# Kernel optimization log

Hardware: AMD Instinct MI355X
Metric: run time of the kernel (lower is better)

Reference implementation:

```python
import jax, jax.numpy as jnp
import numpy as np

N, E, G = 50000, 800000, 64        # nodes, edges, graphs in batch
IN, HID, OUT = 64, 128, 8


def gcn_conv(x, W, b, src, dst, num_nodes):
    """GCNConv: h = D^-1/2 (A+I) D^-1/2 (x W) + b, self-loops already in src/dst."""
    h = x @ W                                              # [N, out]
    deg = jax.ops.segment_sum(jnp.ones_like(dst, dtype=h.dtype), dst,
                              num_segments=num_nodes)      # [N]
    dinv = jax.lax.rsqrt(jnp.maximum(deg, 1.0))
    norm = dinv[src] * dinv[dst]                           # [E+N]
    msg = h[src] * norm[:, None]                           # gather + scale
    out = jax.ops.segment_sum(msg, dst, num_segments=num_nodes)
    return out + b


def global_mean_pool(x, batch, num_graphs):
    s = jax.ops.segment_sum(x, batch, num_segments=num_graphs)
    cnt = jax.ops.segment_sum(jnp.ones((x.shape[0],), x.dtype), batch,
                              num_segments=num_graphs)
    return s / jnp.maximum(cnt, 1.0)[:, None]


def setup_inputs() -> dict:
    key = jax.random.key(0)
    ks = jax.random.split(key, 11)
    def glorot(k, fi, fo):
        return jax.random.normal(k, (fi, fo), jnp.float32) * np.float32(1.0 / np.sqrt(fi))
    return {
        "x": jax.random.normal(ks[0], (N, IN), jnp.float32),
        "W1": glorot(ks[1], IN, HID),  "b1": jnp.zeros((HID,), jnp.float32),
        "W2": glorot(ks[2], HID, HID), "b2": jnp.zeros((HID,), jnp.float32),
        "W3": glorot(ks[3], HID, HID), "b3": jnp.zeros((HID,), jnp.float32),
        "Wh": glorot(ks[4], HID, OUT), "bh": jnp.zeros((OUT,), jnp.float32),
        "edge_index": jax.random.randint(ks[5], (2, E), 0, N),
        "batch": jnp.sort(jax.random.randint(ks[6], (N,), 0, G)),
    }


def reference(x, W1, b1, W2, b2, W3, b3, Wh, bh, edge_index, batch):
    loops = jnp.arange(N, dtype=edge_index.dtype)
    src = jnp.concatenate([edge_index[0], loops])          # add self-loops
    dst = jnp.concatenate([edge_index[1], loops])
    h = jax.nn.relu(gcn_conv(x, W1, b1, src, dst, N))
    h = jax.nn.relu(gcn_conv(h, W2, b2, src, dst, N))
    h = gcn_conv(h, W3, b3, src, dst, N)
    g = global_mean_pool(h, batch, G)                      # [G, HID]
    return g @ Wh + bh                                     # [G, OUT]
```

## Files before the change

kernel.cpp:

```cpp
#include <hip/hip_runtime.h>

typedef short bf8_t __attribute__((ext_vector_type(8)));
typedef float f32x4 __attribute__((ext_vector_type(4)));
typedef unsigned short u16;

__device__ inline u16 f2bf(float f) {
    unsigned u = __float_as_uint(f);
    return (u16)((u + 0x7fff + ((u >> 16) & 1)) >> 16);
}


__global__ void deg_kernel(const int* __restrict__ dst, int* __restrict__ deg,
                           u16* __restrict__ rank, int E) {
    int e = blockIdx.x * 256 + threadIdx.x;
    if (e < E) rank[e] = (u16)atomicAdd(&deg[dst[e]], 1);
}

__global__ void scan_blocksum(const int* __restrict__ deg, int* __restrict__ bsum,
                              float* __restrict__ dinv, int n) {
    int i = blockIdx.x * 256 + threadIdx.x;
    int d = (i < n) ? (deg[i] + 1) : 0;
    if (i < n) dinv[i] = rsqrtf((float)d);
    int v = (i < n) ? ((d + 7) & ~7) : 0;
    for (int off = 32; off > 0; off >>= 1) v += __shfl_down(v, off, 64);
    __shared__ int ws[4];
    if ((threadIdx.x & 63) == 0) ws[threadIdx.x >> 6] = v;
    __syncthreads();
    if (threadIdx.x == 0) bsum[blockIdx.x] = ws[0] + ws[1] + ws[2] + ws[3];
}

__global__ void scan_offsets(const int* __restrict__ bsum, int* __restrict__ boff, int nblk) {
    __shared__ int buf[256];
    int tid = threadIdx.x;
    int v = (tid < nblk) ? bsum[tid] : 0;
    buf[tid] = v;
    __syncthreads();
    for (int off = 1; off < 256; off <<= 1) {
        int t = (tid >= off) ? buf[tid - off] : 0;
        __syncthreads();
        buf[tid] += t;
        __syncthreads();
    }
    if (tid < nblk) boff[tid] = buf[tid] - v;
}

__global__ void scan_rowptr(const int* __restrict__ deg, const int* __restrict__ boff,
                            int* __restrict__ row_ptr, int n) {
    __shared__ int buf[256];
    int tid = threadIdx.x;
    int i = blockIdx.x * 256 + tid;
    int v = (i < n) ? ((deg[i] + 8) & ~7) : 0;
    buf[tid] = v;
    __syncthreads();
    for (int off = 1; off < 256; off <<= 1) {
        int t = (tid >= off) ? buf[tid - off] : 0;
        __syncthreads();
        buf[tid] += t;
        __syncthreads();
    }
    int excl = buf[tid] - v + boff[blockIdx.x];
    if (i < n) row_ptr[i] = excl;
    if (i == n - 1) row_ptr[n] = excl + v;
}


__global__ void prep_kernel(const int* __restrict__ src, const int* __restrict__ dst,
                            const u16* __restrict__ rank, const int* __restrict__ row_ptr,
                            const int* __restrict__ deg,
                            u16* __restrict__ csr_src,
                            const float* __restrict__ x, const float* __restrict__ dinv,
                            unsigned* __restrict__ x16, unsigned* __restrict__ h16a,
                            unsigned* __restrict__ h16b,
                            const float* __restrict__ W1, const float* __restrict__ W2,
                            const float* __restrict__ W3,
                            u16* __restrict__ Wt1, u16* __restrict__ Wt2,
                            u16* __restrict__ Wt3,
                            int E, int n, int total8) {
    int gid = blockIdx.x * 256 + threadIdx.x;
    if (gid < E) {
        int s = src[gid], d = dst[gid];
        int pos = row_ptr[d] + 1 + (int)rank[gid];
        __builtin_nontemporal_store((u16)s, &csr_src[pos]);
        return;
    }
    if (gid < E + n) {
        int s = gid - E;
        int beg = row_ptr[s];
        csr_src[beg] = (u16)s;
        int fill0 = beg + deg[s] + 1, fill1 = row_ptr[s + 1];
        for (int p = fill0; p < fill1; ++p) csr_src[p] = (u16)n;
        return;
    }
    int i = gid - (E + n);
    if (i < total8) {
        float dn = dinv[i >> 3];
        const float4* x4 = (const float4*)x;
        float4 a = x4[i * 2], b = x4[i * 2 + 1];
        uint4 o;
        o.x = (unsigned)f2bf(a.x * dn) | ((unsigned)f2bf(a.y * dn) << 16);
        o.y = (unsigned)f2bf(a.z * dn) | ((unsigned)f2bf(a.w * dn) << 16);
        o.z = (unsigned)f2bf(b.x * dn) | ((unsigned)f2bf(b.y * dn) << 16);
        o.w = (unsigned)f2bf(b.z * dn) | ((unsigned)f2bf(b.w * dn) << 16);
        ((uint4*)x16)[i] = o;
        return;
    }
    int j = i - total8;
    if (j < 8192) {
        int nn = j / 64, k = j - nn * 64;
        Wt1[j] = f2bf(W1[k * 128 + nn]);
        return;
    }
    if (j < 24576) {
        int jj = j - 8192;
        int nn = jj / 128, k = jj - nn * 128;
        Wt2[jj] = f2bf(W2[k * 128 + nn]);
        return;
    }
    if (j < 40960) {
        int jj = j - 24576;
        int nn = jj / 128, k = jj - nn * 128;
        Wt3[jj] = f2bf(W3[k * 128 + nn]);
        return;
    }
    int z = j - 40960;
    if (z < 8)       x16 [(size_t)n * 32 + z]  = 0u;
    else if (z < 16) ((uint4*)x16)[(size_t)n * 8 + (z - 8)] = make_uint4(0,0,0,0);
    else if (z < 32) ((uint4*)h16a)[(size_t)n * 16 + (z - 16)] = make_uint4(0,0,0,0);
    else if (z < 48) ((uint4*)h16b)[(size_t)n * 16 + (z - 32)] = make_uint4(0,0,0,0);
}


__device__ inline void bf8_add(uint4 a, float* acc) {
#pragma unroll
    for (int j = 0; j < 4; ++j) {
        unsigned u = ((const unsigned*)&a)[j];
        acc[2 * j]     += __uint_as_float(u << 16);
        acc[2 * j + 1] += __uint_as_float(u & 0xffff0000u);
    }
}

__device__ inline uint4 pack_bf8(const float* v, float dn) {
    uint4 o;
    o.x = (unsigned)f2bf(v[0] * dn) | ((unsigned)f2bf(v[1] * dn) << 16);
    o.y = (unsigned)f2bf(v[2] * dn) | ((unsigned)f2bf(v[3] * dn) << 16);
    o.z = (unsigned)f2bf(v[4] * dn) | ((unsigned)f2bf(v[5] * dn) << 16);
    o.w = (unsigned)f2bf(v[6] * dn) | ((unsigned)f2bf(v[7] * dn) << 16);
    return o;
}

template<int K, bool RELU, bool BF16OUT>
__global__ __launch_bounds__(256) void agg_gemm(
        const u16* __restrict__ in, const u16* __restrict__ Wt16,
        const float* __restrict__ bias, void* __restrict__ outp,
        const int* __restrict__ row_ptr, const u16* __restrict__ csr_src,
        const float* __restrict__ dinv, int n) {
    constexpr int KS = K / 32;
    __shared__ u16 As[16 * K];
    int w = threadIdx.x >> 6, lane = threadIdx.x & 63;
    int base = blockIdx.x * 16;
    int lr = lane & 15, lk = lane >> 4;

    bf8_t B[2][KS];
#pragma unroll
    for (int f = 0; f < 2; ++f) {
        int col = w * 32 + f * 16 + lr;
#pragma unroll
        for (int ks = 0; ks < KS; ++ks)
            B[f][ks] = *reinterpret_cast<const bf8_t*>(&Wt16[(size_t)col * K + ks * 32 + lk * 8]);
    }

    const uint4* in4 = (const uint4*)in;
    int g = lane >> 4;
    int row = w * 4 + g;
    int node = base + row;
    float acc[8] = {0.f, 0.f, 0.f, 0.f, 0.f, 0.f, 0.f, 0.f};

    if (K == 128) {
        int col = lane & 15;
        if (node < n) {
            int beg = row_ptr[node];
            int niter = (row_ptr[node + 1] - beg) >> 3;
            const uint4* idxp = (const uint4*)(csr_src + beg);
            uint4 iv = idxp[0];
            for (int it = 0; it < niter; ++it) {
                uint4 ivn = idxp[it + 1];
                int s0 = iv.x & 0xffff, s1 = iv.x >> 16;
                int s2 = iv.y & 0xffff, s3 = iv.y >> 16;
                int s4 = iv.z & 0xffff, s5 = iv.z >> 16;
                int s6 = iv.w & 0xffff, s7 = iv.w >> 16;
                uint4 a0 = in4[(size_t)s0 * 16 + col];
                uint4 a1 = in4[(size_t)s1 * 16 + col];
                uint4 a2 = in4[(size_t)s2 * 16 + col];
                uint4 a3 = in4[(size_t)s3 * 16 + col];
                bf8_add(a0, acc); bf8_add(a1, acc);
                bf8_add(a2, acc); bf8_add(a3, acc);
                uint4 a4 = in4[(size_t)s4 * 16 + col];
                uint4 a5 = in4[(size_t)s5 * 16 + col];
                uint4 a6 = in4[(size_t)s6 * 16 + col];
                uint4 a7 = in4[(size_t)s7 * 16 + col];
                bf8_add(a4, acc); bf8_add(a5, acc);
                bf8_add(a6, acc); bf8_add(a7, acc);
                iv = ivn;
            }
        }
        float dn = (node < n) ? dinv[node] : 0.f;
        int off = row * K + ((col * 8) ^ ((row & 7) << 3));
        *(uint4*)&As[off] = pack_bf8(acc, dn);
    } else {
        int sub = (lane >> 3) & 1;
        int col = lane & 7;
        if (node < n) {
            int beg = row_ptr[node];
            int niter = (row_ptr[node + 1] - beg) >> 3;
            const uint4* idxp = (const uint4*)(csr_src + beg);
            uint4 iv = idxp[0];
            for (int it = 0; it < niter; ++it) {
                uint4 ivn = idxp[it + 1];
                int e0 = sub ? (int)(iv.x >> 16) : (int)(iv.x & 0xffff);
                int e1 = sub ? (int)(iv.y >> 16) : (int)(iv.y & 0xffff);
                int e2 = sub ? (int)(iv.z >> 16) : (int)(iv.z & 0xffff);
                int e3 = sub ? (int)(iv.w >> 16) : (int)(iv.w & 0xffff);
                uint4 a0 = in4[(size_t)e0 * 8 + col];
                uint4 a1 = in4[(size_t)e1 * 8 + col];
                uint4 a2 = in4[(size_t)e2 * 8 + col];
                uint4 a3 = in4[(size_t)e3 * 8 + col];
                bf8_add(a0, acc); bf8_add(a1, acc);
                bf8_add(a2, acc); bf8_add(a3, acc);
                iv = ivn;
            }
        }
#pragma unroll
        for (int j = 0; j < 8; ++j)
            acc[j] += __shfl_xor(acc[j], 8, 64);
        if (sub == 0) {
            float dn = (node < n) ? dinv[node] : 0.f;
            int off = row * K + ((col * 8) ^ ((row & 7) << 3));
            *(uint4*)&As[off] = pack_bf8(acc, dn);
        }
    }
    __syncthreads();

    f32x4 pacc[2] = {};
#pragma unroll
    for (int ks = 0; ks < KS; ++ks) {
        int off = lr * K + (((ks * 32) + lk * 8) ^ ((lr & 7) << 3));
        bf8_t a = *reinterpret_cast<const bf8_t*>(&As[off]);
#pragma unroll
        for (int f = 0; f < 2; ++f)
            pacc[f] = __builtin_amdgcn_mfma_f32_16x16x32_bf16(B[f][ks], a, pacc[f], 0, 0, 0);
    }

    int orow = base + lr;
    if (orow < n) {
        float dnx = BF16OUT ? dinv[orow] : 1.f;
#pragma unroll
        for (int f = 0; f < 2; ++f) {
            int c0 = w * 32 + f * 16 + lk * 4;
            float4 bv = *(const float4*)&bias[c0];
            float v0 = pacc[f][0] + bv.x, v1 = pacc[f][1] + bv.y;
            float v2 = pacc[f][2] + bv.z, v3 = pacc[f][3] + bv.w;
            if (RELU) {
                v0 = fmaxf(v0, 0.f); v1 = fmaxf(v1, 0.f);
                v2 = fmaxf(v2, 0.f); v3 = fmaxf(v3, 0.f);
            }
            if (BF16OUT) {
                uint2 o;
                o.x = (unsigned)f2bf(v0 * dnx) | ((unsigned)f2bf(v1 * dnx) << 16);
                o.y = (unsigned)f2bf(v2 * dnx) | ((unsigned)f2bf(v3 * dnx) << 16);
                *(uint2*)&((u16*)outp)[(size_t)orow * 128 + c0] = o;
            } else {
                *(float4*)&((float*)outp)[(size_t)orow * 128 + c0] = make_float4(v0, v1, v2, v3);
            }
        }
    }
}


__device__ inline int lbound(const int* __restrict__ batch, int n, int g) {
    int lo = 0, hi = n;
    while (lo < hi) {
        int mid = (lo + hi) >> 1;
        if (batch[mid] < g) lo = mid + 1; else hi = mid;
    }
    return lo;
}

#define PSPLIT 16
__global__ __launch_bounds__(256) void pool_part(
        const float* __restrict__ h, const int* __restrict__ batch,
        float* __restrict__ part, int n) {
    int g = blockIdx.x >> 4, sp = blockIdx.x & (PSPLIT - 1);
    int tid = threadIdx.x;
    int c = tid & 127, rs = tid >> 7;
    int beg = lbound(batch, n, g), end = lbound(batch, n, g + 1);
    int len = end - beg;
    int chunk = (len + PSPLIT - 1) >> 4;
    int r0 = beg + sp * chunk;
    int r1 = min(r0 + chunk, end);
    float acc = 0.f;
    for (int r = r0 + rs; r < r1; r += 2)
        acc += h[(size_t)r * 128 + c];
    __shared__ float buf[256];
    buf[tid] = acc;
    __syncthreads();
    if (rs == 0)
        part[(size_t)blockIdx.x * 128 + c] = buf[c] + buf[c + 128];
}

__global__ __launch_bounds__(128) void pool_head(
        const float* __restrict__ part, const int* __restrict__ batch,
        const float* __restrict__ Wh, const float* __restrict__ bh,
        float* __restrict__ out, int n) {
    int g = blockIdx.x;
    int tid = threadIdx.x;
    float acc = 0.f;
#pragma unroll
    for (int sp = 0; sp < PSPLIT; ++sp)
        acc += part[((size_t)g * PSPLIT + sp) * 128 + tid];
    int cnt = lbound(batch, n, g + 1) - lbound(batch, n, g);
    __shared__ float grow[128];
    grow[tid] = acc / fmaxf((float)cnt, 1.f);
    __syncthreads();
    int sub = tid >> 3, o = tid & 7;
    float p = 0.f;
    for (int k = sub; k < 128; k += 16)
        p += grow[k] * Wh[k * 8 + o];
    __shared__ float p2[128];
    p2[tid] = p;
    __syncthreads();
    for (int s = 8; s > 0; s >>= 1) {
        if (sub < s) p2[sub * 8 + o] += p2[(sub + s) * 8 + o];
        __syncthreads();
    }
    if (tid < 8) out[g * 8 + tid] = p2[tid] + bh[tid];
}


extern "C" void kernel_launch(void* const* d_in, const int* in_sizes, int n_in,
                              void* d_out, int out_size, void* d_ws, size_t ws_size,
                              hipStream_t stream) {
    const float* x  = (const float*)d_in[0];
    const float* W1 = (const float*)d_in[1];
    const float* b1 = (const float*)d_in[2];
    const float* W2 = (const float*)d_in[3];
    const float* b2 = (const float*)d_in[4];
    const float* W3 = (const float*)d_in[5];
    const float* b3 = (const float*)d_in[6];
    const float* Wh = (const float*)d_in[7];
    const float* bh = (const float*)d_in[8];
    const int* edge_index = (const int*)d_in[9];
    const int* batch = (const int*)d_in[10];
    (void)n_in; (void)ws_size;

    const int N = in_sizes[10];
    const int E = in_sizes[9] / 2;
    const int G = out_size / 8;
    const int* esrc = edge_index;
    const int* edst = edge_index + E;

    size_t off = 0;
    auto take = [&](size_t bytes) {
        void* p = (char*)d_ws + off;
        off += (bytes + 255) & ~(size_t)255;
        return p;
    };
    int*   deg      = (int*)take((size_t)N * 4);
    float* dinv     = (float*)take((size_t)N * 4);
    int*   row_ptr  = (int*)take((size_t)(N + 1) * 4);
    u16*   rank     = (u16*)take((size_t)E * 2);
    u16*   csr_src  = (u16*)take(((size_t)E + 8 * (size_t)N + 16) * 2);
    int*   bsum     = (int*)take(256 * 4);
    int*   boff     = (int*)take(256 * 4);
    float* part     = (float*)take((size_t)G * PSPLIT * 128 * 4);
    u16*   x16      = (u16*)take((size_t)(N + 1) * 64 * 2);
    u16*   h16a     = (u16*)take((size_t)(N + 1) * 128 * 2);
    u16*   h16b     = (u16*)take((size_t)(N + 1) * 128 * 2);
    u16*   Wt1      = (u16*)take((size_t)128 * 64 * 2);
    u16*   Wt2      = (u16*)take((size_t)128 * 128 * 2);
    u16*   Wt3      = (u16*)take((size_t)128 * 128 * 2);
    float* bufA     = (float*)take((size_t)N * 128 * 4);

    int nblk  = (N + 255) / 256;
    int fgrid = (N + 15) / 16;
    int total8 = N * 64 / 8;
    int prep_threads = E + N + total8 + 40960 + 64;

    hipMemsetAsync(deg, 0, (size_t)N * 4, stream);

    deg_kernel<<<(E + 255) / 256, 256, 0, stream>>>(edst, deg, rank, E);
    scan_blocksum<<<nblk, 256, 0, stream>>>(deg, bsum, dinv, N);
    scan_offsets<<<1, 256, 0, stream>>>(bsum, boff, nblk);
    scan_rowptr<<<nblk, 256, 0, stream>>>(deg, boff, row_ptr, N);
    prep_kernel<<<(prep_threads + 255) / 256, 256, 0, stream>>>(
        esrc, edst, rank, row_ptr, deg, csr_src, x, dinv,
        (unsigned*)x16, (unsigned*)h16a, (unsigned*)h16b,
        W1, W2, W3, Wt1, Wt2, Wt3, E, N, total8);

    agg_gemm<64,  true,  true ><<<fgrid, 256, 0, stream>>>(x16,  Wt1, b1, h16a, row_ptr, csr_src, dinv, N);
    agg_gemm<128, true,  true ><<<fgrid, 256, 0, stream>>>(h16a, Wt2, b2, h16b, row_ptr, csr_src, dinv, N);
    agg_gemm<128, false, false><<<fgrid, 256, 0, stream>>>(h16b, Wt3, b3, bufA, row_ptr, csr_src, dinv, N);

    pool_part<<<G * PSPLIT, 256, 0, stream>>>(bufA, batch, part, N);
    pool_head<<<G, 128, 0, stream>>>(part, batch, Wh, bh, (float*)d_out, N);
}
```

Before: 199.9 us.

## Fold layer-3 weight into head and replace final agg-GEMM with aggregation only

Since layer 3 has no activation and is followed by linear mean pooling and the head, W3 and Wh (and b3 into bh) are pre-multiplied into a 128x8 matrix. The last layer becomes a plain sparse aggregation that writes bf16 instead of fp32, and pooling reads bf16. This removes one dense MFMA GEMM and halves the final-layer write and pool read traffic. The cost is one extra bf16 rounding of the aggregated features and a small serial dot-product setup in the prep kernel.

```diff
diff --git a/kernel.cpp b/kernel.cpp
--- a/kernel.cpp
+++ b/kernel.cpp
@@ -73,8 +73,10 @@
                             unsigned* __restrict__ h16b,
                             const float* __restrict__ W1, const float* __restrict__ W2,
                             const float* __restrict__ W3,
+                            const float* __restrict__ Wh, const float* __restrict__ b3,
+                            const float* __restrict__ bh,
                             u16* __restrict__ Wt1, u16* __restrict__ Wt2,
-                            u16* __restrict__ Wt3,
+                            float* __restrict__ WhF, float* __restrict__ bhF,
                             int E, int n, int total8) {
     int gid = blockIdx.x * 256 + threadIdx.x;
     if (gid < E) {
@@ -116,17 +118,27 @@
         Wt2[jj] = f2bf(W2[k * 128 + nn]);
         return;
     }
-    if (j < 40960) {
+    if (j < 25600) {
         int jj = j - 24576;
-        int nn = jj / 128, k = jj - nn * 128;
-        Wt3[jj] = f2bf(W3[k * 128 + nn]);
-        return;
-    }
-    int z = j - 40960;
-    if (z < 8)       x16 [(size_t)n * 32 + z]  = 0u;
-    else if (z < 16) ((uint4*)x16)[(size_t)n * 8 + (z - 8)] = make_uint4(0,0,0,0);
-    else if (z < 32) ((uint4*)h16a)[(size_t)n * 16 + (z - 16)] = make_uint4(0,0,0,0);
-    else if (z < 48) ((uint4*)h16b)[(size_t)n * 16 + (z - 32)] = make_uint4(0,0,0,0);
+        int k = jj >> 3, o = jj & 7;
+        float a = 0.f;
+        for (int q = 0; q < 128; ++q)
+            a += W3[k * 128 + q] * Wh[q * 8 + o];
+        WhF[jj] = a;
+        return;
+    }
+    if (j < 25608) {
+        int o = j - 25600;
+        float a = bh[o];
+        for (int q = 0; q < 128; ++q)
+            a += b3[q] * Wh[q * 8 + o];
+        bhF[o] = a;
+        return;
+    }
+    int z = j - 25608;
+    if (z < 8)       ((uint4*)x16) [(size_t)n * 8  + z]        = make_uint4(0, 0, 0, 0);
+    else if (z < 24) ((uint4*)h16a)[(size_t)n * 16 + (z - 8)]  = make_uint4(0, 0, 0, 0);
+    else if (z < 40) ((uint4*)h16b)[(size_t)n * 16 + (z - 24)] = make_uint4(0, 0, 0, 0);
 }
 
 
@@ -147,6 +159,7 @@
     o.w = (unsigned)f2bf(v[6] * dn) | ((unsigned)f2bf(v[7] * dn) << 16);
     return o;
 }
+
 
 template<int K, bool RELU, bool BF16OUT>
 __global__ __launch_bounds__(256) void agg_gemm(
@@ -276,6 +289,45 @@
 }
 
 
+__global__ __launch_bounds__(256) void agg_only(
+        const u16* __restrict__ in, u16* __restrict__ out,
+        const int* __restrict__ row_ptr, const u16* __restrict__ csr_src,
+        const float* __restrict__ dinv, int n) {
+    int lane = threadIdx.x & 63;
+    int w = threadIdx.x >> 6;
+    int node = blockIdx.x * 16 + w * 4 + (lane >> 4);
+    int col = lane & 15;
+    if (node >= n) return;
+    const uint4* in4 = (const uint4*)in;
+    float acc[8] = {0.f, 0.f, 0.f, 0.f, 0.f, 0.f, 0.f, 0.f};
+    int beg = row_ptr[node];
+    int niter = (row_ptr[node + 1] - beg) >> 3;
+    const uint4* idxp = (const uint4*)(csr_src + beg);
+    uint4 iv = idxp[0];
+    for (int it = 0; it < niter; ++it) {
+        uint4 ivn = idxp[it + 1];
+        int s0 = iv.x & 0xffff, s1 = iv.x >> 16;
+        int s2 = iv.y & 0xffff, s3 = iv.y >> 16;
+        int s4 = iv.z & 0xffff, s5 = iv.z >> 16;
+        int s6 = iv.w & 0xffff, s7 = iv.w >> 16;
+        uint4 a0 = in4[(size_t)s0 * 16 + col];
+        uint4 a1 = in4[(size_t)s1 * 16 + col];
+        uint4 a2 = in4[(size_t)s2 * 16 + col];
+        uint4 a3 = in4[(size_t)s3 * 16 + col];
+        bf8_add(a0, acc); bf8_add(a1, acc);
+        bf8_add(a2, acc); bf8_add(a3, acc);
+        uint4 a4 = in4[(size_t)s4 * 16 + col];
+        uint4 a5 = in4[(size_t)s5 * 16 + col];
+        uint4 a6 = in4[(size_t)s6 * 16 + col];
+        uint4 a7 = in4[(size_t)s7 * 16 + col];
+        bf8_add(a4, acc); bf8_add(a5, acc);
+        bf8_add(a6, acc); bf8_add(a7, acc);
+        iv = ivn;
+    }
+    ((uint4*)out)[(size_t)node * 16 + col] = pack_bf8(acc, dinv[node]);
+}
+
+
 __device__ inline int lbound(const int* __restrict__ batch, int n, int g) {
     int lo = 0, hi = n;
     while (lo < hi) {
@@ -287,29 +339,38 @@
 
 #define PSPLIT 16
 __global__ __launch_bounds__(256) void pool_part(
-        const float* __restrict__ h, const int* __restrict__ batch,
+        const u16* __restrict__ v, const int* __restrict__ batch,
         float* __restrict__ part, int n) {
     int g = blockIdx.x >> 4, sp = blockIdx.x & (PSPLIT - 1);
     int tid = threadIdx.x;
-    int c = tid & 127, rs = tid >> 7;
+    int c2 = tid & 63;
+    int rs = tid >> 6;
     int beg = lbound(batch, n, g), end = lbound(batch, n, g + 1);
     int len = end - beg;
     int chunk = (len + PSPLIT - 1) >> 4;
     int r0 = beg + sp * chunk;
     int r1 = min(r0 + chunk, end);
-    float acc = 0.f;
-    for (int r = r0 + rs; r < r1; r += 2)
-        acc += h[(size_t)r * 128 + c];
-    __shared__ float buf[256];
-    buf[tid] = acc;
-    __syncthreads();
-    if (rs == 0)
-        part[(size_t)blockIdx.x * 128 + c] = buf[c] + buf[c + 128];
+    const unsigned* v32 = (const unsigned*)v;
+    float ax = 0.f, ay = 0.f;
+    for (int r = r0 + rs; r < r1; r += 4) {
+        unsigned u = v32[(size_t)r * 64 + c2];
+        ax += __uint_as_float(u << 16);
+        ay += __uint_as_float(u & 0xffff0000u);
+    }
+    __shared__ float bufx[256], bufy[256];
+    bufx[tid] = ax; bufy[tid] = ay;
+    __syncthreads();
+    if (rs == 0) {
+        float sx = bufx[c2] + bufx[c2 + 64] + bufx[c2 + 128] + bufx[c2 + 192];
+        float sy = bufy[c2] + bufy[c2 + 64] + bufy[c2 + 128] + bufy[c2 + 192];
+        part[(size_t)blockIdx.x * 128 + c2 * 2]     = sx;
+        part[(size_t)blockIdx.x * 128 + c2 * 2 + 1] = sy;
+    }
 }
 
 __global__ __launch_bounds__(128) void pool_head(
         const float* __restrict__ part, const int* __restrict__ batch,
-        const float* __restrict__ Wh, const float* __restrict__ bh,
+        const float* __restrict__ WhF, const float* __restrict__ bhF,
         float* __restrict__ out, int n) {
     int g = blockIdx.x;
     int tid = threadIdx.x;
@@ -324,7 +385,7 @@
     int sub = tid >> 3, o = tid & 7;
     float p = 0.f;
     for (int k = sub; k < 128; k += 16)
-        p += grow[k] * Wh[k * 8 + o];
+        p += grow[k] * WhF[k * 8 + o];
     __shared__ float p2[128];
     p2[tid] = p;
     __syncthreads();
@@ -332,7 +393,7 @@
         if (sub < s) p2[sub * 8 + o] += p2[(sub + s) * 8 + o];
         __syncthreads();
     }
-    if (tid < 8) out[g * 8 + tid] = p2[tid] + bh[tid];
+    if (tid < 8) out[g * 8 + tid] = p2[tid] + bhF[tid];
 }
 
 
@@ -375,15 +436,16 @@
     u16*   x16      = (u16*)take((size_t)(N + 1) * 64 * 2);
     u16*   h16a     = (u16*)take((size_t)(N + 1) * 128 * 2);
     u16*   h16b     = (u16*)take((size_t)(N + 1) * 128 * 2);
+    u16*   vbuf     = (u16*)take((size_t)N * 128 * 2);
     u16*   Wt1      = (u16*)take((size_t)128 * 64 * 2);
     u16*   Wt2      = (u16*)take((size_t)128 * 128 * 2);
-    u16*   Wt3      = (u16*)take((size_t)128 * 128 * 2);
-    float* bufA     = (float*)take((size_t)N * 128 * 4);
+    float* WhF      = (float*)take((size_t)128 * 8 * 4);
+    float* bhF      = (float*)take(8 * 4);
 
     int nblk  = (N + 255) / 256;
     int fgrid = (N + 15) / 16;
     int total8 = N * 64 / 8;
-    int prep_threads = E + N + total8 + 40960 + 64;
+    int prep_threads = E + N + total8 + 25608 + 40;
 
     hipMemsetAsync(deg, 0, (size_t)N * 4, stream);
 
@@ -394,12 +456,12 @@
     prep_kernel<<<(prep_threads + 255) / 256, 256, 0, stream>>>(
         esrc, edst, rank, row_ptr, deg, csr_src, x, dinv,
         (unsigned*)x16, (unsigned*)h16a, (unsigned*)h16b,
-        W1, W2, W3, Wt1, Wt2, Wt3, E, N, total8);
-
-    agg_gemm<64,  true,  true ><<<fgrid, 256, 0, stream>>>(x16,  Wt1, b1, h16a, row_ptr, csr_src, dinv, N);
-    agg_gemm<128, true,  true ><<<fgrid, 256, 0, stream>>>(h16a, Wt2, b2, h16b, row_ptr, csr_src, dinv, N);
-    agg_gemm<128, false, false><<<fgrid, 256, 0, stream>>>(h16b, Wt3, b3, bufA, row_ptr, csr_src, dinv, N);
-
-    pool_part<<<G * PSPLIT, 256, 0, stream>>>(bufA, batch, part, N);
-    pool_head<<<G, 128, 0, stream>>>(part, batch, Wh, bh, (float*)d_out, N);
-}
+        W1, W2, W3, Wh, b3, bh, Wt1, Wt2, WhF, bhF, E, N, total8);
+
+    agg_gemm<64,  true, true><<<fgrid, 256, 0, stream>>>(x16,  Wt1, b1, h16a, row_ptr, csr_src, dinv, N);
+    agg_gemm<128, true, true><<<fgrid, 256, 0, stream>>>(h16a, Wt2, b2, h16b, row_ptr, csr_src, dinv, N);
+    agg_only<<<fgrid, 256, 0, stream>>>(h16b, vbuf, row_ptr, csr_src, dinv, N);
+
+    pool_part<<<G * PSPLIT, 256, 0, stream>>>(vbuf, batch, part, N);
+    pool_head<<<G, 128, 0, stream>>>(part, batch, WhF, bhF, (float*)d_out, N);
+}
```

Result: faster. 189.0 us (median of 2 runs) (-5.5%).
